# Optimization experiments

Hardware: AMD Instinct MI355X
Metric: run time of the kernel (lower is better)

The kernel has to match this reference:

```python
import jax, jax.numpy as jnp
import numpy as np

B, IN_DIM, OUT_DIM = 16384, 1024, 512
N_CAPS, CAP_DIM = 8, 16


def squash(x, axis=-1):
    # scale = |x|^2 / (1 + |x|^2) ; out = scale * x / sqrt(|x|^2 + 1e-8)
    sq = jnp.sum(x * x, axis=axis, keepdims=True)
    return (sq / (1.0 + sq)) * x / jnp.sqrt(sq + 1e-8)


def setup_inputs() -> dict:
    key = jax.random.key(0)
    k1, k2, k3, k4 = jax.random.split(key, 4)
    x = jax.random.normal(k1, (B, IN_DIM), dtype=jnp.float32)
    # Linear(in_dim, n_caps*cap_dim) params (kaiming-ish scale)
    Wp = jax.random.normal(k2, (IN_DIM, N_CAPS * CAP_DIM), dtype=jnp.float32) / np.sqrt(IN_DIM)
    bp = jax.random.normal(k3, (N_CAPS * CAP_DIM,), dtype=jnp.float32) * 0.01
    # routing transform W: [n_caps, cap_dim, out_dim], init std 0.02 as in torch code
    W = jax.random.normal(k4, (N_CAPS, CAP_DIM, OUT_DIM), dtype=jnp.float32) * 0.02
    return {"x": x, "Wp": Wp, "bp": bp, "W": W, "n_routing": 3}


def reference(x, Wp, bp, W, n_routing):
    batch = x.shape[0]
    primary = x @ Wp + bp                                   # [B, n*d]
    primary = primary.reshape(batch, N_CAPS, CAP_DIM)       # [B, n, d]
    primary = squash(primary, axis=-1)
    u_hat = jnp.einsum('bnd,ndo->bno', primary, W)          # [B, n, o]
    b = jnp.zeros((batch, N_CAPS, 1), dtype=x.dtype)
    v = None
    for i in range(n_routing):
        c = jax.nn.softmax(b, axis=1)                       # [B, n, 1]
        s = jnp.sum(c * u_hat, axis=1)                      # [B, o]
        v = squash(s, axis=-1)                              # [B, o]
        if i < n_routing - 1:
            agreement = jnp.einsum('bno,bo->bn', u_hat, v)  # [B, n]
            b = b + agreement[..., None]
    return v
```

## Files before the change

### kernel.cpp

```cpp
#include <hip/hip_runtime.h>
#include <hip/hip_bf16.h>
#include <math.h>

typedef __attribute__((ext_vector_type(8))) short bf16x8;
typedef __attribute__((ext_vector_type(8))) unsigned short u16x8;
typedef __attribute__((ext_vector_type(4))) float f32x4;
typedef __attribute__((ext_vector_type(16))) float f32x16;

__device__ __forceinline__ unsigned short f2bf(float f) {
  unsigned u = __float_as_uint(f);
  return (unsigned short)((u + 0x7FFFu + ((u >> 16) & 1u)) >> 16);
}
__device__ __forceinline__ float bf2f(unsigned short h) {
  return __uint_as_float(((unsigned)h) << 16);
}
__device__ __forceinline__ void cvt8pk_a(const float* f, u16x8& h, u16x8& l) {
  unsigned* hp = (unsigned*)&h;
  unsigned* lp = (unsigned*)&l;
#pragma unroll
  for (int i = 0; i < 4; ++i) {
    __hip_bfloat162 hb = __float22bfloat162_rn(make_float2(f[2*i], f[2*i+1]));
    unsigned hv = *(unsigned*)&hb;
    hp[i] = hv;
    float r0 = f[2*i]     - __uint_as_float(hv << 16);
    float r1 = f[2*i + 1] - __uint_as_float(hv & 0xFFFF0000u);
    __hip_bfloat162 lb = __float22bfloat162_rn(make_float2(r0, r1));
    lp[i] = *(unsigned*)&lb;
  }
}
__device__ __forceinline__ void cvt8pk(const float4& a, const float4& b,
                                       u16x8& h, u16x8& l) {
  float f[8] = {a.x, a.y, a.z, a.w, b.x, b.y, b.z, b.w};
  cvt8pk_a(f, h, l);
}
__device__ __forceinline__ void cvt8b(const float4& a, const float4& b,
                                      bf16x8& h, bf16x8& l) {
  u16x8 hh, ll;
  cvt8pk(a, b, hh, ll);
  h = *(bf16x8*)&hh;
  l = *(bf16x8*)&ll;
}

#define GLD16(g, l) __builtin_amdgcn_global_load_lds( \
    (const __attribute__((address_space(1))) void*)(g), \
    (__attribute__((address_space(3))) void*)(l), 16, 0, 0)

#define MFMA16(a, b, c) __builtin_amdgcn_mfma_f32_16x16x32_bf16(a, b, c, 0, 0, 0)
#define MFMA32(a, b, c) __builtin_amdgcn_mfma_f32_32x32x16_bf16(a, b, c, 0, 0, 0)

__global__ __launch_bounds__(256) void caps_prep_all(
    const float* __restrict__ Wp, const float* __restrict__ W,
    unsigned short* __restrict__ th1, unsigned short* __restrict__ tl1,
    unsigned short* __restrict__ th2, unsigned short* __restrict__ tl2,
    unsigned short* __restrict__ th3, unsigned short* __restrict__ tl3)
{
  __shared__ float tile[64][128];
  const int t = threadIdx.x, b = blockIdx.x;
  if (b < 16) {
    const float* src = Wp + (size_t)b * 64 * 128;
#pragma unroll
    for (int i = 0; i < 8; ++i) {
      int j = t + i * 256;
      int kk = j >> 5, q = j & 31;
      *(float4*)&tile[kk][q * 4] = *(const float4*)(src + kk * 128 + q * 4);
    }
    __syncthreads();
    const int col = t >> 1, kg0 = (t & 1) * 4;
    unsigned short hi[32], lo[32];
#pragma unroll
    for (int kk = 0; kk < 32; ++kk) {
      float v = tile[kg0 * 8 + kk][col];
      unsigned short h = f2bf(v);
      hi[kk] = h;
      lo[kk] = f2bf(v - bf2f(h));
    }
#pragma unroll
    for (int i = 0; i < 4; ++i) {
      size_t off = (size_t)b * 8192 + (size_t)(kg0 + i) * 1024 + (size_t)col * 8;
      u16x8 vh, vl;
#pragma unroll
      for (int e = 0; e < 8; ++e) { vh[e] = hi[i * 8 + e]; vl[e] = lo[i * 8 + e]; }
      *(u16x8*)(th1 + off) = vh;
      *(u16x8*)(tl1 + off) = vl;
    }
  } else if (b < 32) {
    int tt = (b - 16) * 256 + t;
#pragma unroll
    for (int h = 0; h < 2; ++h) {
      int c = tt + h * 4096;
      int kt = c >> 12, rem = c & 4095;
      int kg = rem >> 9, col = rem & 511;
      int kbase = kt * 64 + kg * 8;
      u16x8 vh, vl;
#pragma unroll
      for (int e = 0; e < 8; ++e) {
        float v = W[(size_t)(kbase + e) * 512 + col];
        unsigned short hh = f2bf(v);
        vh[e] = hh;
        vl[e] = f2bf(v - bf2f(hh));
      }
      size_t off = ((size_t)(kt * 8 + kg) * 512 + col) * 8;
      *(u16x8*)(th2 + off) = vh;
      *(u16x8*)(tl2 + off) = vl;
    }
  } else {
    int bb = b - 32;
    int a = (bb >> 3) * 16 + (t >> 4);
    int c = (bb & 7) * 16 + (t & 15);
    const float* wa = W + (size_t)a * 512;
    const float* wb = W + (size_t)c * 512;
    float acc = 0.f;
#pragma unroll 4
    for (int o = 0; o < 512; o += 4) {
      float4 xx = *(const float4*)(wa + o);
      float4 yy = *(const float4*)(wb + o);
      acc += xx.x * yy.x + xx.y * yy.y + xx.z * yy.z + xx.w * yy.w;
    }
    unsigned short h = f2bf(acc);
    unsigned short l = f2bf(acc - bf2f(h));
    size_t off = ((size_t)(a >> 3) * 128 + c) * 8 + (a & 7);
    th3[off] = h;
    tl3[off] = l;
  }
}

__global__ __launch_bounds__(256) void caps_primary(
    const float* __restrict__ x, const unsigned short* __restrict__ bth,
    const unsigned short* __restrict__ btl, const float* __restrict__ bp,
    float* __restrict__ p_out)
{
  __shared__ unsigned short lds[18432];
  const int tid  = threadIdx.x;
  const int lane = tid & 63;
  const int w    = tid >> 6;
  const int cb   = lane & 15;
  const int kgl  = lane >> 4;
  const int row0 = blockIdx.x * 16;

  const int rowA = (tid & 127) >> 3;
  const int kgA  = tid & 7;
  const float* xrow = x + (size_t)(row0 + rowA) * 1024 + kgA * 8;

  f32x4 acc[2];
  acc[0] = (f32x4){0.f, 0.f, 0.f, 0.f};
  acc[1] = (f32x4){0.f, 0.f, 0.f, 0.f};

  for (int kt = 0; kt < 16; ++kt) {
    {
      const unsigned short* gh = bth + (size_t)kt * 8192 + (size_t)tid * 8;
      const unsigned short* gl = btl + (size_t)kt * 8192 + (size_t)tid * 8;
#pragma unroll
      for (int c = 0; c < 4; ++c) {
        GLD16(gh + c * 2048, lds + 2048  + (c * 256 + tid) * 8);
        GLD16(gl + c * 2048, lds + 10240 + (c * 256 + tid) * 8);
      }
    }
    if (tid < 128) {
      const float* xp = xrow + kt * 64;
      float4 a0 = *(const float4*)(xp);
      float4 a1 = *(const float4*)(xp + 4);
      u16x8 h_, l_;
      cvt8pk(a0, a1, h_, l_);
      *(u16x8*)(lds + (kgA * 16 + rowA) * 8) = h_;
      *(u16x8*)(lds + 1024 + (kgA * 16 + rowA) * 8) = l_;
    }
    __syncthreads();

#pragma unroll
    for (int s = 0; s < 2; ++s) {
      const int ks = s * 4 + kgl;
      bf16x8 ah = *(const bf16x8*)(lds + (ks * 16 + cb) * 8);
      bf16x8 al = *(const bf16x8*)(lds + 1024 + (ks * 16 + cb) * 8);
#pragma unroll
      for (int nf = 0; nf < 2; ++nf) {
        const int col = w * 32 + nf * 16 + cb;
        bf16x8 bh  = *(const bf16x8*)(lds + 2048  + (ks * 128 + col) * 8);
        bf16x8 blo = *(const bf16x8*)(lds + 10240 + (ks * 128 + col) * 8);
        acc[nf] = MFMA16(ah, bh,  acc[nf]);
        acc[nf] = MFMA16(ah, blo, acc[nf]);
        acc[nf] = MFMA16(al, bh,  acc[nf]);
      }
    }
    __syncthreads();
  }

  const int l4 = lane >> 4;
#pragma unroll
  for (int nf = 0; nf < 2; ++nf) {
    const int col = w * 32 + nf * 16 + cb;
    const float bpv = bp[col];
#pragma unroll
    for (int r = 0; r < 4; ++r) {
      float val = acc[nf][r] + bpv;
      float sq = val * val;
      sq += __shfl_xor(sq, 1); sq += __shfl_xor(sq, 2);
      sq += __shfl_xor(sq, 4); sq += __shfl_xor(sq, 8);
      float sc = (sq / (1.f + sq)) / sqrtf(sq + 1e-8f);
      p_out[(size_t)(row0 + l4 * 4 + r) * 128 + col] = val * sc;
    }
  }
}

__global__ __launch_bounds__(512) void caps_route_g(
    const float* __restrict__ p_in, const unsigned short* __restrict__ mh,
    const unsigned short* __restrict__ ml, float* __restrict__ cs_out)
{
  __shared__ float pT[128 * 65];
  __shared__ unsigned short Msh[32768];
  __shared__ float t_lds[64 * 9];
  __shared__ float c_lds[64 * 9];
  const int tid  = threadIdx.x;
  const int lane = tid & 63;
  const int w    = tid >> 6;
  const int wm   = w >> 2;
  const int wn   = w & 3;
  const int lc   = lane & 31;
  const int hi   = lane >> 5;
  const int row0 = blockIdx.x * 64;

#pragma unroll
  for (int i = 0; i < 4; ++i) {
    int idx = tid + i * 512;
    *(u16x8*)&Msh[idx * 8] = *(const u16x8*)(mh + (size_t)idx * 8);
    *(u16x8*)&Msh[16384 + idx * 8] = *(const u16x8*)(ml + (size_t)idx * 8);
  }
#pragma unroll
  for (int i = 0; i < 4; ++i) {
    int j = tid + i * 512;
    int r = j >> 5, c4 = j & 31;
    f32x4 v = *(const f32x4*)(p_in + (size_t)(row0 + r) * 128 + c4 * 4);
    pT[(c4 * 4 + 0) * 65 + r] = v[0];
    pT[(c4 * 4 + 1) * 65 + r] = v[1];
    pT[(c4 * 4 + 2) * 65 + r] = v[2];
    pT[(c4 * 4 + 3) * 65 + r] = v[3];
  }
  if (w == 0) {
#pragma unroll
    for (int n = 0; n < 8; ++n) c_lds[lane * 9 + n] = 0.125f;
  }
  __syncthreads();

  const int arow = wm * 32 + lc;
  const int col  = wn * 32 + lc;
  const int cap  = wn * 2 + (lc >> 4);
  float bb[8] = {0.f, 0.f, 0.f, 0.f, 0.f, 0.f, 0.f, 0.f};

#pragma unroll 1
  for (int it = 0; it < 3; ++it) {
    f32x16 acc;
#pragma unroll
    for (int j = 0; j < 16; ++j) acc[j] = 0.f;

#pragma unroll
    for (int kk = 0; kk < 8; ++kk) {
      const float cv = c_lds[arow * 9 + kk];
      float q[8];
#pragma unroll
      for (int e = 0; e < 8; ++e)
        q[e] = pT[(kk * 16 + hi * 8 + e) * 65 + arow] * cv;
      u16x8 hq, lq;
      cvt8pk_a(q, hq, lq);
      const int fi = ((kk * 2 + hi) * 128 + col) * 8;
      bf16x8 mbh = *(const bf16x8*)&Msh[fi];
      bf16x8 mbl = *(const bf16x8*)&Msh[16384 + fi];
      acc = MFMA32(*(bf16x8*)&hq, mbh, acc);
      acc = MFMA32(*(bf16x8*)&hq, mbl, acc);
      acc = MFMA32(*(bf16x8*)&lq, mbh, acc);
    }

    float tp[16];
#pragma unroll
    for (int r = 0; r < 16; ++r) {
      const int row = wm * 32 + (r & 3) + 8 * (r >> 2) + 4 * hi;
      float prod = pT[col * 65 + row] * acc[r];
      prod += __shfl_xor(prod, 1);
      prod += __shfl_xor(prod, 2);
      prod += __shfl_xor(prod, 4);
      prod += __shfl_xor(prod, 8);
      tp[r] = prod;
    }
    __syncthreads();
    if ((lc & 15) == 0) {
#pragma unroll
      for (int r = 0; r < 16; ++r) {
        const int row = wm * 32 + (r & 3) + 8 * (r >> 2) + 4 * hi;
        t_lds[row * 9 + cap] = tp[r];
      }
    }
    __syncthreads();

    if (w == 0) {
      float c[8], t[8];
#pragma unroll
      for (int n = 0; n < 8; ++n) {
        c[n] = c_lds[lane * 9 + n];
        t[n] = t_lds[lane * 9 + n];
      }
      float ss = 0.f;
#pragma unroll
      for (int n = 0; n < 8; ++n) ss = fmaf(c[n], t[n], ss);
      float scale = (ss / (1.f + ss)) / sqrtf(ss + 1e-8f);
      if (it < 2) {
#pragma unroll
        for (int n = 0; n < 8; ++n) bb[n] += scale * t[n];
        float mx = bb[0];
#pragma unroll
        for (int n = 1; n < 8; ++n) mx = fmaxf(mx, bb[n]);
        float e[8], Z = 0.f;
#pragma unroll
        for (int n = 0; n < 8; ++n) { e[n] = expf(bb[n] - mx); Z += e[n]; }
        float inv = 1.f / Z;
#pragma unroll
        for (int n = 0; n < 8; ++n) c_lds[lane * 9 + n] = e[n] * inv;
      } else {
        f32x4 c0 = {scale * c[0], scale * c[1], scale * c[2], scale * c[3]};
        f32x4 c1 = {scale * c[4], scale * c[5], scale * c[6], scale * c[7]};
        *(f32x4*)(cs_out + (size_t)(row0 + lane) * 8)     = c0;
        *(f32x4*)(cs_out + (size_t)(row0 + lane) * 8 + 4) = c1;
      }
    }
    __syncthreads();
  }
}

__global__ __launch_bounds__(512) void caps_vout(
    const float* __restrict__ p, const unsigned short* __restrict__ bth,
    const unsigned short* __restrict__ btl, const float* __restrict__ cs,
    float* __restrict__ out)
{
  __shared__ unsigned short Bsh[32768];
  const int tid  = threadIdx.x;
  const int lane = tid & 63;
  const int w    = tid >> 6;
  const int wm   = w >> 2;
  const int wn   = w & 3;
  const int lc   = lane & 31;
  const int hi   = lane >> 5;
  const int row0 = blockIdx.x * 64;
  const int col0 = blockIdx.y * 128;

#pragma unroll
  for (int i = 0; i < 4; ++i) {
    int idx = tid + i * 512;
    int kt = idx >> 10, kg = (idx >> 7) & 7, col = idx & 127;
    size_t g = ((size_t)(kt * 8 + kg) * 512 + col0 + col) * 8;
    *(u16x8*)&Bsh[idx * 8] = *(const u16x8*)(bth + g);
    *(u16x8*)&Bsh[16384 + idx * 8] = *(const u16x8*)(btl + g);
  }

  const int rA = row0 + wm * 32 + lc;
  const float* qp = p + (size_t)rA * 128;
  float cs8[8];
  *(f32x4*)&cs8[0] = *(const f32x4*)(cs + (size_t)rA * 8);
  *(f32x4*)&cs8[4] = *(const f32x4*)(cs + (size_t)rA * 8 + 4);
  __syncthreads();

  f32x16 acc;
#pragma unroll
  for (int j = 0; j < 16; ++j) acc[j] = 0.f;

#pragma unroll
  for (int kt = 0; kt < 2; ++kt) {
#pragma unroll
    for (int kk = 0; kk < 4; ++kk) {
      const float* qk = qp + kt * 64 + kk * 16 + hi * 8;
      float4 a0 = *(const float4*)(qk);
      float4 a1 = *(const float4*)(qk + 4);
      const float cv = cs8[kt * 4 + kk];
      a0.x *= cv; a0.y *= cv; a0.z *= cv; a0.w *= cv;
      a1.x *= cv; a1.y *= cv; a1.z *= cv; a1.w *= cv;
      bf16x8 ah, al;
      cvt8b(a0, a1, ah, al);
      const int ks = kk * 2 + hi;
      const int fi = ((kt * 8 + ks) * 128 + wn * 32 + lc) * 8;
      bf16x8 bh  = *(const bf16x8*)&Bsh[fi];
      bf16x8 blo = *(const bf16x8*)&Bsh[16384 + fi];
      acc = MFMA32(ah, bh,  acc);
      acc = MFMA32(ah, blo, acc);
      acc = MFMA32(al, bh,  acc);
    }
  }

#pragma unroll
  for (int r = 0; r < 16; ++r) {
    const int row = (r & 3) + 8 * (r >> 2) + 4 * hi;
    out[(size_t)(row0 + wm * 32 + row) * 512 + col0 + wn * 32 + lc] = acc[r];
  }
}

extern "C" void kernel_launch(void* const* d_in, const int* in_sizes, int n_in,
                              void* d_out, int out_size, void* d_ws, size_t ws_size,
                              hipStream_t stream) {
  (void)in_sizes; (void)n_in; (void)out_size; (void)ws_size;
  const float* x  = (const float*)d_in[0];
  const float* Wp = (const float*)d_in[1];
  const float* bp = (const float*)d_in[2];
  const float* W  = (const float*)d_in[3];
  char* ws = (char*)d_ws;
  float* p_ws = (float*)ws;
  unsigned short* th1 = (unsigned short*)(ws + 8388608);
  unsigned short* tl1 = (unsigned short*)(ws + 8650752);
  unsigned short* th2 = (unsigned short*)(ws + 8912896);
  unsigned short* tl2 = (unsigned short*)(ws + 9043968);
  unsigned short* th3 = (unsigned short*)(ws + 9175040);
  unsigned short* tl3 = (unsigned short*)(ws + 9207808);
  float* cs_ws = (float*)(ws + 9240576);
  float* outp = (float*)d_out;

  caps_prep_all<<<96, 256, 0, stream>>>(Wp, W, th1, tl1, th2, tl2, th3, tl3);
  caps_primary<<<1024, 256, 0, stream>>>(x, th1, tl1, bp, p_ws);
  caps_route_g<<<256, 512, 0, stream>>>(p_ws, th3, tl3, cs_ws);
  caps_vout<<<dim3(256, 4), 512, 0, stream>>>(p_ws, th2, tl2, cs_ws, outp);
}
```

Before: 93.77 us.

## Retile primary projection GEMM to 64-row blocks with 32x32 MFMA

Measured after the change: 90.43 us. 3.6% less time.

```diff
diff --git a/kernel.cpp b/kernel.cpp
--- a/kernel.cpp
+++ b/kernel.cpp
@@ -45,7 +45,6 @@
     (const __attribute__((address_space(1))) void*)(g), \
     (__attribute__((address_space(3))) void*)(l), 16, 0, 0)
 
-#define MFMA16(a, b, c) __builtin_amdgcn_mfma_f32_16x16x32_bf16(a, b, c, 0, 0, 0)
 #define MFMA32(a, b, c) __builtin_amdgcn_mfma_f32_32x32x16_bf16(a, b, c, 0, 0, 0)
 
 __global__ __launch_bounds__(256) void caps_prep_all(
@@ -124,80 +123,81 @@
   }
 }
 
-__global__ __launch_bounds__(256) void caps_primary(
+__global__ __launch_bounds__(512) void caps_primary(
     const float* __restrict__ x, const unsigned short* __restrict__ bth,
     const unsigned short* __restrict__ btl, const float* __restrict__ bp,
     float* __restrict__ p_out)
 {
-  __shared__ unsigned short lds[18432];
+  __shared__ unsigned short lds[49152];
   const int tid  = threadIdx.x;
   const int lane = tid & 63;
   const int w    = tid >> 6;
-  const int cb   = lane & 15;
-  const int kgl  = lane >> 4;
-  const int row0 = blockIdx.x * 16;
-
-  const int rowA = (tid & 127) >> 3;
-  const int kgA  = tid & 7;
-  const float* xrow = x + (size_t)(row0 + rowA) * 1024 + kgA * 8;
-
-  f32x4 acc[2];
-  acc[0] = (f32x4){0.f, 0.f, 0.f, 0.f};
-  acc[1] = (f32x4){0.f, 0.f, 0.f, 0.f};
-
-  for (int kt = 0; kt < 16; ++kt) {
+  const int wm   = w >> 2;
+  const int wn   = w & 3;
+  const int lc   = lane & 31;
+  const int hi   = lane >> 5;
+  const int row0 = blockIdx.x * 64;
+
+  const int colB = wn * 32 + lc;
+  const int rowA = tid & 63;
+  const int kgA0 = tid >> 6;
+  const float* xrow = x + (size_t)(row0 + rowA) * 1024;
+
+  f32x16 acc;
+#pragma unroll
+  for (int j = 0; j < 16; ++j) acc[j] = 0.f;
+
+#pragma unroll 1
+  for (int KT = 0; KT < 8; ++KT) {
     {
-      const unsigned short* gh = bth + (size_t)kt * 8192 + (size_t)tid * 8;
-      const unsigned short* gl = btl + (size_t)kt * 8192 + (size_t)tid * 8;
+      const unsigned short* gh = bth + (size_t)KT * 16384 + (size_t)tid * 8;
+      const unsigned short* gl = btl + (size_t)KT * 16384 + (size_t)tid * 8;
 #pragma unroll
       for (int c = 0; c < 4; ++c) {
-        GLD16(gh + c * 2048, lds + 2048  + (c * 256 + tid) * 8);
-        GLD16(gl + c * 2048, lds + 10240 + (c * 256 + tid) * 8);
+        GLD16(gh + c * 4096, lds + 16384 + (c * 512 + tid) * 8);
+        GLD16(gl + c * 4096, lds + 32768 + (c * 512 + tid) * 8);
       }
     }
-    if (tid < 128) {
-      const float* xp = xrow + kt * 64;
-      float4 a0 = *(const float4*)(xp);
-      float4 a1 = *(const float4*)(xp + 4);
-      u16x8 h_, l_;
-      cvt8pk(a0, a1, h_, l_);
-      *(u16x8*)(lds + (kgA * 16 + rowA) * 8) = h_;
-      *(u16x8*)(lds + 1024 + (kgA * 16 + rowA) * 8) = l_;
-    }
-    __syncthreads();
-
-#pragma unroll
-    for (int s = 0; s < 2; ++s) {
-      const int ks = s * 4 + kgl;
-      bf16x8 ah = *(const bf16x8*)(lds + (ks * 16 + cb) * 8);
-      bf16x8 al = *(const bf16x8*)(lds + 1024 + (ks * 16 + cb) * 8);
-#pragma unroll
-      for (int nf = 0; nf < 2; ++nf) {
-        const int col = w * 32 + nf * 16 + cb;
-        bf16x8 bh  = *(const bf16x8*)(lds + 2048  + (ks * 128 + col) * 8);
-        bf16x8 blo = *(const bf16x8*)(lds + 10240 + (ks * 128 + col) * 8);
-        acc[nf] = MFMA16(ah, bh,  acc[nf]);
-        acc[nf] = MFMA16(ah, blo, acc[nf]);
-        acc[nf] = MFMA16(al, bh,  acc[nf]);
-      }
-    }
-    __syncthreads();
-  }
-
-  const int l4 = lane >> 4;
-#pragma unroll
-  for (int nf = 0; nf < 2; ++nf) {
-    const int col = w * 32 + nf * 16 + cb;
-    const float bpv = bp[col];
-#pragma unroll
-    for (int r = 0; r < 4; ++r) {
-      float val = acc[nf][r] + bpv;
-      float sq = val * val;
-      sq += __shfl_xor(sq, 1); sq += __shfl_xor(sq, 2);
-      sq += __shfl_xor(sq, 4); sq += __shfl_xor(sq, 8);
-      float sc = (sq / (1.f + sq)) / sqrtf(sq + 1e-8f);
-      p_out[(size_t)(row0 + l4 * 4 + r) * 128 + col] = val * sc;
-    }
+    {
+      const float* xp = xrow + KT * 128;
+      float4 a0 = *(const float4*)(xp + kgA0 * 8);
+      float4 a1 = *(const float4*)(xp + kgA0 * 8 + 4);
+      float4 a2 = *(const float4*)(xp + (kgA0 + 8) * 8);
+      float4 a3 = *(const float4*)(xp + (kgA0 + 8) * 8 + 4);
+      u16x8 h0, l0, h1, l1;
+      cvt8pk(a0, a1, h0, l0);
+      cvt8pk(a2, a3, h1, l1);
+      *(u16x8*)(lds + (kgA0 * 64 + rowA) * 8) = h0;
+      *(u16x8*)(lds + 8192 + (kgA0 * 64 + rowA) * 8) = l0;
+      *(u16x8*)(lds + ((kgA0 + 8) * 64 + rowA) * 8) = h1;
+      *(u16x8*)(lds + 8192 + ((kgA0 + 8) * 64 + rowA) * 8) = l1;
+    }
+    __syncthreads();
+
+#pragma unroll
+    for (int kk = 0; kk < 8; ++kk) {
+      const int ks = kk * 2 + hi;
+      bf16x8 ah  = *(const bf16x8*)(lds + (ks * 64 + wm * 32 + lc) * 8);
+      bf16x8 al  = *(const bf16x8*)(lds + 8192 + (ks * 64 + wm * 32 + lc) * 8);
+      bf16x8 bh  = *(const bf16x8*)(lds + 16384 + (ks * 128 + colB) * 8);
+      bf16x8 blo = *(const bf16x8*)(lds + 32768 + (ks * 128 + colB) * 8);
+      acc = MFMA32(ah, bh,  acc);
+      acc = MFMA32(ah, blo, acc);
+      acc = MFMA32(al, bh,  acc);
+    }
+    __syncthreads();
+  }
+
+  const float bpv = bp[colB];
+#pragma unroll
+  for (int r = 0; r < 16; ++r) {
+    const int row = wm * 32 + (r & 3) + 8 * (r >> 2) + 4 * hi;
+    float val = acc[r] + bpv;
+    float sq = val * val;
+    sq += __shfl_xor(sq, 1); sq += __shfl_xor(sq, 2);
+    sq += __shfl_xor(sq, 4); sq += __shfl_xor(sq, 8);
+    float sc = (sq / (1.f + sq)) / sqrtf(sq + 1e-8f);
+    p_out[(size_t)(row0 + row) * 128 + colB] = val * sc;
   }
 }
 
@@ -408,7 +408,7 @@
   float* outp = (float*)d_out;
 
   caps_prep_all<<<96, 256, 0, stream>>>(Wp, W, th1, tl1, th2, tl2, th3, tl3);
-  caps_primary<<<1024, 256, 0, stream>>>(x, th1, tl1, bp, p_ws);
+  caps_primary<<<256, 512, 0, stream>>>(x, th1, tl1, bp, p_ws);
   caps_route_g<<<256, 512, 0, stream>>>(p_ws, th3, tl3, cs_ws);
   caps_vout<<<dim3(256, 4), 512, 0, stream>>>(p_ws, th2, tl2, cs_ws, outp);
 }
```
